# Optimization experiments

Hardware: AMD Instinct MI355X
Metric: run time of the kernel (lower is better)

Reference implementation:

```python
import jax, jax.numpy as jnp
import numpy as np

B, T, E, A = 8, 2048, 1024, 1024


def setup_inputs() -> dict:
    key = jax.random.key(0)
    k1, k2, k3, k4 = jax.random.split(key, 4)
    embedded = jax.random.normal(k1, (B, T, E), dtype=jnp.float32)
    s = 1.0 / np.sqrt(E)
    # nn.Linear(E, A, bias=False) stores weight of shape (A, E); y = x @ W^T
    Wq = jax.random.uniform(k2, (A, E), dtype=jnp.float32, minval=-s, maxval=s)
    Wk = jax.random.uniform(k3, (A, E), dtype=jnp.float32, minval=-s, maxval=s)
    Wv = jax.random.uniform(k4, (A, E), dtype=jnp.float32, minval=-s, maxval=s)
    return {"embedded": embedded, "Wq": Wq, "Wk": Wk, "Wv": Wv}


def reference(embedded, Wq, Wk, Wv):
    # q, k, v: [B, T, A]
    q = jnp.einsum("bte,ae->bta", embedded, Wq)
    k = jnp.einsum("bte,ae->bta", embedded, Wk)
    v = jnp.einsum("bte,ae->bta", embedded, Wv)
    scale = 1.0 / jnp.sqrt(jnp.asarray(Wq.shape[0], dtype=q.dtype))
    # causal scores: [B, T, T]
    scores = jnp.einsum("bqa,bka->bqk", q, k) * scale
    t = scores.shape[-1]
    causal = jnp.tril(jnp.ones((t, t), dtype=bool))
    scores = jnp.where(causal, scores, jnp.asarray(-jnp.inf, dtype=scores.dtype))
    attn = jax.nn.softmax(scores, axis=-1)
    return jnp.einsum("bqk,bka->bqa", attn, v)
```

## Files before the change

kernel.cpp:

```cpp
#include <hip/hip_runtime.h>
#include <hip/hip_bf16.h>
#include <stdint.h>


#define BB 8
#define TT 2048
#define EE 1024
#define AA 1024
#define MM (BB * TT)

typedef short bf16x8 __attribute__((ext_vector_type(8)));
typedef float f32x4 __attribute__((ext_vector_type(4)));

#define GLOAD_LDS16(g, l)                                                      \
  __builtin_amdgcn_global_load_lds(                                            \
      (const __attribute__((address_space(1))) void*)(g),                      \
      (__attribute__((address_space(3))) void*)(l), 16, 0, 0)

#define SBAR()                               \
  do {                                       \
    __builtin_amdgcn_sched_barrier(0);       \
    __builtin_amdgcn_s_barrier();            \
    __builtin_amdgcn_sched_barrier(0);       \
  } while (0)

#define LGKM0()                                          \
  do {                                                   \
    asm volatile("s_waitcnt lgkmcnt(0)" ::: "memory");   \
    __builtin_amdgcn_sched_barrier(0);                   \
  } while (0)

#define VMCNT(n)                                              \
  do {                                                        \
    asm volatile("s_waitcnt vmcnt(" #n ")" ::: "memory");     \
    __builtin_amdgcn_sched_barrier(0);                        \
  } while (0)

__device__ __forceinline__ void gemm256_core(
    const short* __restrict__ gA, int lda, int a0row,
    const short* __restrict__ gB, int ldb, int b0row, int NT, short* As,
    short* Bs, f32x4 (*acc)[4]) {
  const int tid = threadIdx.x;
  const int lane = tid & 63;
  const int w = tid >> 6;
  const int wr = w >> 2, wc = w & 3;
  const int lrow = lane & 15;
  const int lk8 = (lane >> 4) * 8;
  const int swz = ((lrow >> 3) & 1) << 4;
  const int baseA = (((wr * 128 + lrow) * 32) + lk8) ^ swz;
  const int baseB = (((wc * 64 + lrow) * 32) + lk8) ^ swz;

  const short* pA[2];
  const short* pB[2];
  int dL[2];
#pragma unroll
  for (int i = 0; i < 2; ++i) {
    int chunk = 2 * w + i;
    int P = chunk * 1024 + lane * 16;
    int L = P ^ (((P >> 9) & 1) << 5);
    int row = L >> 6;
    int kb2 = (L & 63) >> 1;
    pA[i] = gA + (size_t)(a0row + row) * lda + kb2;
    pB[i] = gB + (size_t)(b0row + row) * ldb + kb2;
    dL[i] = chunk * 512 + lane * 8;
  }

#define STG_A(tl, s)                                                           \
  do {                                                                         \
    int _o = (tl) * 64 + (s) * 32;                                             \
    short* _d = As + (((tl) & 1) << 14) + ((s) << 13);                         \
    GLOAD_LDS16(pA[0] + _o, _d + dL[0]);                                       \
    GLOAD_LDS16(pA[1] + _o, _d + dL[1]);                                       \
  } while (0)
#define STG_B(tl, s)                                                           \
  do {                                                                         \
    int _o = (tl) * 64 + (s) * 32;                                             \
    short* _d = Bs + (((tl) & 1) << 14) + ((s) << 13);                         \
    GLOAD_LDS16(pB[0] + _o, _d + dL[0]);                                       \
    GLOAD_LDS16(pB[1] + _o, _d + dL[1]);                                       \
  } while (0)

  STG_B(0, 0); STG_A(0, 0); STG_B(0, 1); STG_A(0, 1);
  if (NT > 1) {
    STG_B(1, 0); STG_A(1, 0); STG_A(1, 1);
    VMCNT(6);
  } else {
    VMCNT(0);
  }
  SBAR();

  for (int t = 0; t < NT; ++t) {
    short* Ac = As + (t & 1) * 16384;
    short* Bc = Bs + (t & 1) * 16384;
    const bool stg = (t < NT - 2);
    bf16x8 a0[4], a1[4], a2[4], a3[4], b0[4], b1[4];

#pragma unroll
    for (int m = 0; m < 4; ++m) a0[m] = *(const bf16x8*)&Ac[baseA + m * 512];
#pragma unroll
    for (int n = 0; n < 4; ++n) b0[n] = *(const bf16x8*)&Bc[baseB + n * 512];
    if (t < NT - 1) STG_B(t + 1, 1);
    SBAR();
    LGKM0();
    __builtin_amdgcn_s_setprio(1);
#pragma unroll
    for (int m = 0; m < 4; ++m)
#pragma unroll
      for (int n = 0; n < 4; ++n)
        acc[m][n] = __builtin_amdgcn_mfma_f32_16x16x32_bf16(a0[m], b0[n],
                                                            acc[m][n], 0, 0, 0);
    __builtin_amdgcn_s_setprio(0);
    SBAR();

#pragma unroll
    for (int m = 0; m < 4; ++m)
      a1[m] = *(const bf16x8*)&Ac[baseA + (m + 4) * 512];
#pragma unroll
    for (int m = 0; m < 4; ++m)
      a2[m] = *(const bf16x8*)&Ac[8192 + baseA + m * 512];
    if (stg) STG_B(t + 2, 0);
    SBAR();
    LGKM0();
    __builtin_amdgcn_s_setprio(1);
#pragma unroll
    for (int m = 0; m < 4; ++m)
#pragma unroll
      for (int n = 0; n < 4; ++n)
        acc[m + 4][n] = __builtin_amdgcn_mfma_f32_16x16x32_bf16(
            a1[m], b0[n], acc[m + 4][n], 0, 0, 0);
    __builtin_amdgcn_s_setprio(0);
    SBAR();

#pragma unroll
    for (int m = 0; m < 4; ++m)
      a3[m] = *(const bf16x8*)&Ac[8192 + baseA + (m + 4) * 512];
#pragma unroll
    for (int n = 0; n < 4; ++n)
      b1[n] = *(const bf16x8*)&Bc[8192 + baseB + n * 512];
    if (stg) STG_A(t + 2, 0);
    SBAR();
    LGKM0();
    __builtin_amdgcn_s_setprio(1);
#pragma unroll
    for (int m = 0; m < 4; ++m)
#pragma unroll
      for (int n = 0; n < 4; ++n)
        acc[m][n] = __builtin_amdgcn_mfma_f32_16x16x32_bf16(a2[m], b1[n],
                                                            acc[m][n], 0, 0, 0);
    __builtin_amdgcn_s_setprio(0);
    SBAR();

    if (stg) {
      STG_A(t + 2, 1);
      VMCNT(6);
    } else if (t == NT - 2) {
      VMCNT(0);
    }
    SBAR();
    __builtin_amdgcn_s_setprio(1);
#pragma unroll
    for (int m = 0; m < 4; ++m)
#pragma unroll
      for (int n = 0; n < 4; ++n)
        acc[m + 4][n] = __builtin_amdgcn_mfma_f32_16x16x32_bf16(
            a3[m], b1[n], acc[m + 4][n], 0, 0, 0);
    __builtin_amdgcn_s_setprio(0);
    SBAR();
  }
#undef STG_A
#undef STG_B
}

__global__ __launch_bounds__(512, 2) void qkv_gemm8(
    const short* __restrict__ xb, const short* __restrict__ Wb,
    short* __restrict__ qk, short* __restrict__ Vt) {
  __shared__ __align__(16) short SH[65536];
  short* As = SH;
  short* Bs = SH + 32768;
  int f = blockIdx.x;
  int s = (f & 7) * 96 + (f >> 3);
  int mt = s / 12, nt = s % 12;
  int z = nt >> 2, ntl = nt & 3;
  const short* gB = Wb + (size_t)z * AA * EE + (size_t)(ntl * 256) * EE;
  f32x4 acc[8][4];
#pragma unroll
  for (int m = 0; m < 8; ++m)
#pragma unroll
    for (int n = 0; n < 4; ++n) acc[m][n] = (f32x4){0.f, 0.f, 0.f, 0.f};
  gemm256_core(xb, EE, mt * 256, gB, EE, 0, EE / 64, As, Bs, acc);

  int tid = threadIdx.x;
  int lane = tid & 63, w = tid >> 6, wr = w >> 2, wc = w & 3;
  int lrow = lane & 15, lk4 = (lane >> 4) * 4;

  if (z < 2) {
    short* o = qk + (size_t)z * MM * AA;
    int row0 = mt * 256 + wr * 128;
    int col0 = ntl * 256 + wc * 64;
#pragma unroll
    for (int m = 0; m < 8; ++m)
#pragma unroll
      for (int n = 0; n < 4; ++n)
#pragma unroll
        for (int r = 0; r < 4; ++r) {
          int row = row0 + m * 16 + lk4 + r;
          int col = col0 + n * 16 + lrow;
          __hip_bfloat16 h = __float2bfloat16(acc[m][n][r]);
          o[(size_t)row * AA + col] = *(short*)&h;
        }
  } else {
    __syncthreads();
    int lr0 = wr * 128, lc0 = wc * 64;
#pragma unroll
    for (int m = 0; m < 8; ++m)
#pragma unroll
      for (int n = 0; n < 4; ++n)
#pragma unroll
        for (int r = 0; r < 4; ++r) {
          int lr = lr0 + m * 16 + lk4 + r;
          int lc = lc0 + n * 16 + lrow;
          __hip_bfloat16 h = __float2bfloat16(acc[m][n][r]);
          SH[lc * 256 + (lr ^ ((lc & 7) << 3))] = *(short*)&h;
        }
    __syncthreads();
    int row0 = mt * 256;
    int bq = row0 >> 11;
    int t0 = row0 & 2047;
#pragma unroll
    for (int pass = 0; pass < 4; ++pass) {
      int lc = pass * 64 + (tid >> 3);
      int d = ntl * 256 + lc;
      size_t dst = ((size_t)bq * AA + d) * TT + t0;
      int sw = (lc & 7) << 3;
#pragma unroll
      for (int g = 0; g < 4; ++g) {
        int lr = (tid & 7) * 8 + g * 64;
        bf16x8 vv = *(const bf16x8*)&SH[lc * 256 + (lr ^ sw)];
        *(bf16x8*)&Vt[dst + lr] = vv;
      }
    }
  }
}

__device__ __forceinline__ void stage_tile(const short* __restrict__ g,
                                           size_t stride, short* lds, int tid) {
#pragma unroll
  for (int r = 0; r < 4; ++r) {
    int t = r * 256 + tid;
    int row = t >> 3;
    int c = (t & 7) * 8;
    GLOAD_LDS16(g + (size_t)row * stride + c, lds + (size_t)t * 8);
  }
}

__device__ __forceinline__ void mfma_step(const short* As, const short* Bs,
                                          f32x4 acc[4][4], int lane, int wr,
                                          int wc) {
  int lrow = lane & 15;
  int lk = (lane >> 4) * 8;
#pragma unroll
  for (int kk = 0; kk < 64; kk += 32) {
    bf16x8 a[4], b[4];
#pragma unroll
    for (int i = 0; i < 4; ++i)
      a[i] = *(const bf16x8*)&As[(wr * 64 + i * 16 + lrow) * 64 + kk + lk];
#pragma unroll
    for (int j = 0; j < 4; ++j)
      b[j] = *(const bf16x8*)&Bs[(wc * 64 + j * 16 + lrow) * 64 + kk + lk];
#pragma unroll
    for (int i = 0; i < 4; ++i)
#pragma unroll
      for (int j = 0; j < 4; ++j)
        acc[i][j] =
            __builtin_amdgcn_mfma_f32_16x16x32_bf16(a[i], b[j], acc[i][j], 0, 0, 0);
  }
}

__global__ void prep(const float* __restrict__ x, const float* __restrict__ wq,
                     const float* __restrict__ wk, const float* __restrict__ wv,
                     short* __restrict__ Xb, short* __restrict__ Wb,
                     float* __restrict__ Ls) {
  const int nx4 = MM * EE / 4;
  const int nw4 = AA * EE / 4;
  int gid = blockIdx.x * blockDim.x + threadIdx.x;
  if (gid < MM) Ls[gid] = 0.f;
  int stride = gridDim.x * blockDim.x;
  for (int i = gid; i < nx4 + 3 * nw4; i += stride) {
    const float* src;
    short* dst;
    int ii;
    if (i < nx4) {
      src = x; dst = Xb; ii = i;
    } else {
      int j = i - nx4;
      int z = j / nw4;
      ii = j - z * nw4;
      src = (z == 0) ? wq : (z == 1 ? wk : wv);
      dst = Wb + (size_t)z * AA * EE;
    }
    float4 v = ((const float4*)src)[ii];
    __hip_bfloat16 h0 = __float2bfloat16(v.x);
    __hip_bfloat16 h1 = __float2bfloat16(v.y);
    __hip_bfloat16 h2 = __float2bfloat16(v.z);
    __hip_bfloat16 h3 = __float2bfloat16(v.w);
    short4 o;
    o.x = *(short*)&h0;
    o.y = *(short*)&h1;
    o.z = *(short*)&h2;
    o.w = *(short*)&h3;
    ((short4*)dst)[ii] = o;
  }
}

__global__ __launch_bounds__(256) void score_gemm(const short* __restrict__ Qb,
                                                  const short* __restrict__ Kb,
                                                  short* __restrict__ Pu,
                                                  float* __restrict__ lsum) {
  int f = blockIdx.x;
  int b = f & 7;
  int j = f >> 3;
  int mt = 0;
  while ((mt + 1) * (mt + 2) / 2 <= j) ++mt;
  int nt = j - mt * (mt + 1) / 2;
  int q0 = mt * 128, c0 = nt * 128;

  __shared__ __align__(16) short As[128 * 64];
  __shared__ __align__(16) short Bs[128 * 64];
  int tid = threadIdx.x;
  int lane = tid & 63, wid = tid >> 6, wr = wid >> 1, wc = wid & 1;
  const short* Q = Qb + (size_t)b * TT * AA;
  const short* K = Kb + (size_t)b * TT * AA;
  f32x4 acc[4][4];
#pragma unroll
  for (int i = 0; i < 4; ++i)
#pragma unroll
    for (int jj = 0; jj < 4; ++jj) acc[i][jj] = (f32x4){0.f, 0.f, 0.f, 0.f};

  for (int k0 = 0; k0 < AA; k0 += 64) {
    stage_tile(Q + (size_t)q0 * AA + k0, AA, As, tid);
    stage_tile(K + (size_t)c0 * AA + k0, AA, Bs, tid);
    __syncthreads();
    mfma_step(As, Bs, acc, lane, wr, wc);
    __syncthreads();
  }
  const float scale = 0.03125f;
  short* P = Pu + (size_t)b * TT * TT;
  int lrow = lane & 15, lk4 = (lane >> 4) * 4;
#pragma unroll
  for (int i = 0; i < 4; ++i) {
#pragma unroll
    for (int r = 0; r < 4; ++r) {
      int q = q0 + wr * 64 + i * 16 + lk4 + r;
      float rs = 0.f;
#pragma unroll
      for (int jj = 0; jj < 4; ++jj) {
        int kx = c0 + wc * 64 + jj * 16 + lrow;
        float e = (kx <= q) ? __expf(acc[i][jj][r] * scale) : 0.f;
        rs += e;
        __hip_bfloat16 h = __float2bfloat16(e);
        P[(size_t)q * TT + kx] = *(short*)&h;
      }
      rs += __shfl_xor(rs, 1);
      rs += __shfl_xor(rs, 2);
      rs += __shfl_xor(rs, 4);
      rs += __shfl_xor(rs, 8);
      if (lrow == 0) atomicAdd(&lsum[b * TT + q], rs);
    }
  }
}

__global__ __launch_bounds__(256) void pv_gemm(const short* __restrict__ Pu,
                                               const short* __restrict__ Vt,
                                               const float* __restrict__ lsum,
                                               float* __restrict__ out) {
  int f = blockIdx.x;
  int b = f & 7;
  int j = f >> 3;
  int p = j >> 3;
  int nt = j & 7;
  int n0 = nt * 128;

  __shared__ __align__(16) short As[128 * 64];
  __shared__ __align__(16) short Bs[128 * 64];
  int tid = threadIdx.x;
  int lane = tid & 63, wid = tid >> 6, wr = wid >> 1, wc = wid & 1;
  const short* P = Pu + (size_t)b * TT * TT;
  const short* V = Vt + (size_t)b * AA * TT;
  int lrow = lane & 15, lk4 = (lane >> 4) * 4;

#pragma unroll
  for (int s = 0; s < 2; ++s) {
    int mt = s ? (15 - p) : p;
    int q0 = mt * 128;
    f32x4 acc[4][4];
#pragma unroll
    for (int i = 0; i < 4; ++i)
#pragma unroll
      for (int jj = 0; jj < 4; ++jj) acc[i][jj] = (f32x4){0.f, 0.f, 0.f, 0.f};

    int kend = q0 + 128;
    for (int k0 = 0; k0 < kend; k0 += 64) {
      stage_tile(P + (size_t)q0 * TT + k0, TT, As, tid);
      stage_tile(V + (size_t)n0 * TT + k0, TT, Bs, tid);
      __syncthreads();
      mfma_step(As, Bs, acc, lane, wr, wc);
      __syncthreads();
    }
#pragma unroll
    for (int i = 0; i < 4; ++i) {
#pragma unroll
      for (int r = 0; r < 4; ++r) {
        int q = q0 + wr * 64 + i * 16 + lk4 + r;
        float linv = 1.0f / lsum[b * TT + q];
#pragma unroll
        for (int jj = 0; jj < 4; ++jj) {
          int d = n0 + wc * 64 + jj * 16 + lrow;
          out[((size_t)(b * TT + q)) * AA + d] = acc[i][jj][r] * linv;
        }
      }
    }
  }
}

extern "C" void kernel_launch(void* const* d_in, const int* in_sizes, int n_in,
                              void* d_out, int out_size, void* d_ws,
                              size_t ws_size, hipStream_t stream) {
  const float* x = (const float*)d_in[0];
  const float* Wq = (const float*)d_in[1];
  const float* Wk = (const float*)d_in[2];
  const float* Wv = (const float*)d_in[3];

  char* ws = (char*)d_ws;
  size_t oWb = 0;
  size_t oQb = oWb + (size_t)3 * AA * EE * 2;
  size_t oKb = oQb + (size_t)MM * AA * 2;
  size_t oVt = oKb + (size_t)MM * AA * 2;
  size_t oLs = oVt + (size_t)MM * AA * 2;
  size_t oXb = oLs + (size_t)MM * 4;
  size_t oPu = oXb;

  short* Wb = (short*)(ws + oWb);
  short* Qb = (short*)(ws + oQb);
  short* Kb = (short*)(ws + oKb);
  short* Vt = (short*)(ws + oVt);
  float* Ls = (float*)(ws + oLs);
  short* Xb = (short*)(ws + oXb);
  short* Pu = (short*)(ws + oPu);

  prep<<<2048, 256, 0, stream>>>(x, Wq, Wk, Wv, Xb, Wb, Ls);

  qkv_gemm8<<<768, 512, 0, stream>>>(Xb, Wb, Qb, Vt);
  score_gemm<<<1088, 256, 0, stream>>>(Qb, Kb, Pu, Ls);
  pv_gemm<<<512, 256, 0, stream>>>(Pu, Vt, Ls, (float*)d_out);
}
```

Measured before the change: 260.8 us.

## Split causal score GEMM into 256-tile off-diagonal and 128-tile diagonal kernels

The score computation is split in two. A new 256x256-tile kernel (512 threads, reusing gemm256_core) covers the strictly-below-diagonal blocks without masking, and a 128-tile kernel covers the three lower-triangle sub-tiles of each 256 diagonal block with the causal mask. The PV kernel now computes its paired short and long query tiles in one loop that shares the staged V tile, instead of running two sequential passes. This aims to raise data reuse and MFMA efficiency in the score phase and halve V loads in PV, at the cost of an extra launch and higher register and LDS pressure.

```diff
diff --git a/kernel.cpp b/kernel.cpp
--- a/kernel.cpp
+++ b/kernel.cpp
@@ -242,6 +242,56 @@
   }
 }
 
+__global__ __launch_bounds__(512, 2) void score256(const short* __restrict__ Qb,
+                                                   const short* __restrict__ Kb,
+                                                   short* __restrict__ Pu,
+                                                   float* __restrict__ lsum) {
+  __shared__ __align__(16) short As[32768];
+  __shared__ __align__(16) short Bs[32768];
+  int f = blockIdx.x;
+  int b = f & 7;
+  int j = f >> 3;
+  int MT = 1;
+  while ((MT + 1) * MT / 2 <= j) ++MT;
+  int NT = j - MT * (MT - 1) / 2;
+  const short* Q = Qb + (size_t)b * TT * AA;
+  const short* K = Kb + (size_t)b * TT * AA;
+  f32x4 acc[8][4];
+#pragma unroll
+  for (int m = 0; m < 8; ++m)
+#pragma unroll
+    for (int n = 0; n < 4; ++n) acc[m][n] = (f32x4){0.f, 0.f, 0.f, 0.f};
+  gemm256_core(Q, AA, MT * 256, K, AA, NT * 256, AA / 64, As, Bs, acc);
+
+  const float scale = 0.03125f;
+  short* P = Pu + (size_t)b * TT * TT;
+  int lane = threadIdx.x & 63, w = threadIdx.x >> 6, wr = w >> 2, wc = w & 3;
+  int lrow = lane & 15, lk4 = (lane >> 4) * 4;
+  int q0 = MT * 256 + wr * 128;
+  int c0 = NT * 256 + wc * 64;
+#pragma unroll
+  for (int m = 0; m < 8; ++m) {
+#pragma unroll
+    for (int r = 0; r < 4; ++r) {
+      int q = q0 + m * 16 + lk4 + r;
+      float rs = 0.f;
+#pragma unroll
+      for (int n = 0; n < 4; ++n) {
+        int kx = c0 + n * 16 + lrow;
+        float e = __expf(acc[m][n][r] * scale);
+        rs += e;
+        __hip_bfloat16 h = __float2bfloat16(e);
+        P[(size_t)q * TT + kx] = *(short*)&h;
+      }
+      rs += __shfl_xor(rs, 1);
+      rs += __shfl_xor(rs, 2);
+      rs += __shfl_xor(rs, 4);
+      rs += __shfl_xor(rs, 8);
+      if (lrow == 0) atomicAdd(&lsum[b * TT + q], rs);
+    }
+  }
+}
+
 __device__ __forceinline__ void stage_tile(const short* __restrict__ g,
                                            size_t stride, short* lds, int tid) {
 #pragma unroll
@@ -273,6 +323,125 @@
       for (int j = 0; j < 4; ++j)
         acc[i][j] =
             __builtin_amdgcn_mfma_f32_16x16x32_bf16(a[i], b[j], acc[i][j], 0, 0, 0);
+  }
+}
+
+__global__ __launch_bounds__(256) void score_diag(const short* __restrict__ Qb,
+                                                  const short* __restrict__ Kb,
+                                                  short* __restrict__ Pu,
+                                                  float* __restrict__ lsum) {
+  int f = blockIdx.x;
+  int b = f & 7;
+  int j = f >> 3;
+  int M = j / 3, r3 = j - 3 * M;
+  int mt = 2 * M + (r3 > 0);
+  int nt = 2 * M + (r3 == 2);
+  int q0 = mt * 128, c0 = nt * 128;
+
+  __shared__ __align__(16) short As[128 * 64];
+  __shared__ __align__(16) short Bs[128 * 64];
+  int tid = threadIdx.x;
+  int lane = tid & 63, wid = tid >> 6, wr = wid >> 1, wc = wid & 1;
+  const short* Q = Qb + (size_t)b * TT * AA;
+  const short* K = Kb + (size_t)b * TT * AA;
+  f32x4 acc[4][4];
+#pragma unroll
+  for (int i = 0; i < 4; ++i)
+#pragma unroll
+    for (int jj = 0; jj < 4; ++jj) acc[i][jj] = (f32x4){0.f, 0.f, 0.f, 0.f};
+
+  for (int k0 = 0; k0 < AA; k0 += 64) {
+    stage_tile(Q + (size_t)q0 * AA + k0, AA, As, tid);
+    stage_tile(K + (size_t)c0 * AA + k0, AA, Bs, tid);
+    __syncthreads();
+    mfma_step(As, Bs, acc, lane, wr, wc);
+    __syncthreads();
+  }
+  const float scale = 0.03125f;
+  short* P = Pu + (size_t)b * TT * TT;
+  int lrow = lane & 15, lk4 = (lane >> 4) * 4;
+#pragma unroll
+  for (int i = 0; i < 4; ++i) {
+#pragma unroll
+    for (int r = 0; r < 4; ++r) {
+      int q = q0 + wr * 64 + i * 16 + lk4 + r;
+      float rs = 0.f;
+#pragma unroll
+      for (int jj = 0; jj < 4; ++jj) {
+        int kx = c0 + wc * 64 + jj * 16 + lrow;
+        float e = (kx <= q) ? __expf(acc[i][jj][r] * scale) : 0.f;
+        rs += e;
+        __hip_bfloat16 h = __float2bfloat16(e);
+        P[(size_t)q * TT + kx] = *(short*)&h;
+      }
+      rs += __shfl_xor(rs, 1);
+      rs += __shfl_xor(rs, 2);
+      rs += __shfl_xor(rs, 4);
+      rs += __shfl_xor(rs, 8);
+      if (lrow == 0) atomicAdd(&lsum[b * TT + q], rs);
+    }
+  }
+}
+
+__global__ __launch_bounds__(256) void pv_gemm(const short* __restrict__ Pu,
+                                               const short* __restrict__ Vt,
+                                               const float* __restrict__ lsum,
+                                               float* __restrict__ out) {
+  int f = blockIdx.x;
+  int b = f & 7;
+  int j = f >> 3;
+  int pp = j >> 3;
+  int nt = j & 7;
+  int n0 = nt * 128;
+  int q0A = pp * 128;
+  int q0B = (15 - pp) * 128;
+  int e1 = 2 * (pp + 1);
+  int e2 = 2 * (16 - pp);
+
+  __shared__ __align__(16) short A1[128 * 64];
+  __shared__ __align__(16) short A2[128 * 64];
+  __shared__ __align__(16) short BV[128 * 64];
+  int tid = threadIdx.x;
+  int lane = tid & 63, wid = tid >> 6, wr = wid >> 1, wc = wid & 1;
+  const short* P = Pu + (size_t)b * TT * TT;
+  const short* V = Vt + (size_t)b * AA * TT;
+  int lrow = lane & 15, lk4 = (lane >> 4) * 4;
+
+  f32x4 accA[4][4], accB[4][4];
+#pragma unroll
+  for (int i = 0; i < 4; ++i)
+#pragma unroll
+    for (int jj = 0; jj < 4; ++jj) {
+      accA[i][jj] = (f32x4){0.f, 0.f, 0.f, 0.f};
+      accB[i][jj] = (f32x4){0.f, 0.f, 0.f, 0.f};
+    }
+
+  for (int k = 0; k < e2; ++k) {
+    int k0 = k * 64;
+    stage_tile(V + (size_t)n0 * TT + k0, TT, BV, tid);
+    stage_tile(P + (size_t)q0B * TT + k0, TT, A2, tid);
+    if (k < e1) stage_tile(P + (size_t)q0A * TT + k0, TT, A1, tid);
+    __syncthreads();
+    mfma_step(A2, BV, accB, lane, wr, wc);
+    if (k < e1) mfma_step(A1, BV, accA, lane, wr, wc);
+    __syncthreads();
+  }
+
+#pragma unroll
+  for (int i = 0; i < 4; ++i) {
+#pragma unroll
+    for (int r = 0; r < 4; ++r) {
+      int qA = q0A + wr * 64 + i * 16 + lk4 + r;
+      int qB = q0B + wr * 64 + i * 16 + lk4 + r;
+      float lA = 1.0f / lsum[b * TT + qA];
+      float lB = 1.0f / lsum[b * TT + qB];
+#pragma unroll
+      for (int jj = 0; jj < 4; ++jj) {
+        int d = n0 + wc * 64 + jj * 16 + lrow;
+        out[((size_t)(b * TT + qA)) * AA + d] = accA[i][jj][r] * lA;
+        out[((size_t)(b * TT + qB)) * AA + d] = accB[i][jj][r] * lB;
+      }
+    }
   }
 }
 
@@ -312,116 +481,6 @@
   }
 }
 
-__global__ __launch_bounds__(256) void score_gemm(const short* __restrict__ Qb,
-                                                  const short* __restrict__ Kb,
-                                                  short* __restrict__ Pu,
-                                                  float* __restrict__ lsum) {
-  int f = blockIdx.x;
-  int b = f & 7;
-  int j = f >> 3;
-  int mt = 0;
-  while ((mt + 1) * (mt + 2) / 2 <= j) ++mt;
-  int nt = j - mt * (mt + 1) / 2;
-  int q0 = mt * 128, c0 = nt * 128;
-
-  __shared__ __align__(16) short As[128 * 64];
-  __shared__ __align__(16) short Bs[128 * 64];
-  int tid = threadIdx.x;
-  int lane = tid & 63, wid = tid >> 6, wr = wid >> 1, wc = wid & 1;
-  const short* Q = Qb + (size_t)b * TT * AA;
-  const short* K = Kb + (size_t)b * TT * AA;
-  f32x4 acc[4][4];
-#pragma unroll
-  for (int i = 0; i < 4; ++i)
-#pragma unroll
-    for (int jj = 0; jj < 4; ++jj) acc[i][jj] = (f32x4){0.f, 0.f, 0.f, 0.f};
-
-  for (int k0 = 0; k0 < AA; k0 += 64) {
-    stage_tile(Q + (size_t)q0 * AA + k0, AA, As, tid);
-    stage_tile(K + (size_t)c0 * AA + k0, AA, Bs, tid);
-    __syncthreads();
-    mfma_step(As, Bs, acc, lane, wr, wc);
-    __syncthreads();
-  }
-  const float scale = 0.03125f;
-  short* P = Pu + (size_t)b * TT * TT;
-  int lrow = lane & 15, lk4 = (lane >> 4) * 4;
-#pragma unroll
-  for (int i = 0; i < 4; ++i) {
-#pragma unroll
-    for (int r = 0; r < 4; ++r) {
-      int q = q0 + wr * 64 + i * 16 + lk4 + r;
-      float rs = 0.f;
-#pragma unroll
-      for (int jj = 0; jj < 4; ++jj) {
-        int kx = c0 + wc * 64 + jj * 16 + lrow;
-        float e = (kx <= q) ? __expf(acc[i][jj][r] * scale) : 0.f;
-        rs += e;
-        __hip_bfloat16 h = __float2bfloat16(e);
-        P[(size_t)q * TT + kx] = *(short*)&h;
-      }
-      rs += __shfl_xor(rs, 1);
-      rs += __shfl_xor(rs, 2);
-      rs += __shfl_xor(rs, 4);
-      rs += __shfl_xor(rs, 8);
-      if (lrow == 0) atomicAdd(&lsum[b * TT + q], rs);
-    }
-  }
-}
-
-__global__ __launch_bounds__(256) void pv_gemm(const short* __restrict__ Pu,
-                                               const short* __restrict__ Vt,
-                                               const float* __restrict__ lsum,
-                                               float* __restrict__ out) {
-  int f = blockIdx.x;
-  int b = f & 7;
-  int j = f >> 3;
-  int p = j >> 3;
-  int nt = j & 7;
-  int n0 = nt * 128;
-
-  __shared__ __align__(16) short As[128 * 64];
-  __shared__ __align__(16) short Bs[128 * 64];
-  int tid = threadIdx.x;
-  int lane = tid & 63, wid = tid >> 6, wr = wid >> 1, wc = wid & 1;
-  const short* P = Pu + (size_t)b * TT * TT;
-  const short* V = Vt + (size_t)b * AA * TT;
-  int lrow = lane & 15, lk4 = (lane >> 4) * 4;
-
-#pragma unroll
-  for (int s = 0; s < 2; ++s) {
-    int mt = s ? (15 - p) : p;
-    int q0 = mt * 128;
-    f32x4 acc[4][4];
-#pragma unroll
-    for (int i = 0; i < 4; ++i)
-#pragma unroll
-      for (int jj = 0; jj < 4; ++jj) acc[i][jj] = (f32x4){0.f, 0.f, 0.f, 0.f};
-
-    int kend = q0 + 128;
-    for (int k0 = 0; k0 < kend; k0 += 64) {
-      stage_tile(P + (size_t)q0 * TT + k0, TT, As, tid);
-      stage_tile(V + (size_t)n0 * TT + k0, TT, Bs, tid);
-      __syncthreads();
-      mfma_step(As, Bs, acc, lane, wr, wc);
-      __syncthreads();
-    }
-#pragma unroll
-    for (int i = 0; i < 4; ++i) {
-#pragma unroll
-      for (int r = 0; r < 4; ++r) {
-        int q = q0 + wr * 64 + i * 16 + lk4 + r;
-        float linv = 1.0f / lsum[b * TT + q];
-#pragma unroll
-        for (int jj = 0; jj < 4; ++jj) {
-          int d = n0 + wc * 64 + jj * 16 + lrow;
-          out[((size_t)(b * TT + q)) * AA + d] = acc[i][jj][r] * linv;
-        }
-      }
-    }
-  }
-}
-
 extern "C" void kernel_launch(void* const* d_in, const int* in_sizes, int n_in,
                               void* d_out, int out_size, void* d_ws,
                               size_t ws_size, hipStream_t stream) {
@@ -450,6 +509,7 @@
   prep<<<2048, 256, 0, stream>>>(x, Wq, Wk, Wv, Xb, Wb, Ls);
 
   qkv_gemm8<<<768, 512, 0, stream>>>(Xb, Wb, Qb, Vt);
-  score_gemm<<<1088, 256, 0, stream>>>(Qb, Kb, Pu, Ls);
+  score256<<<224, 512, 0, stream>>>(Qb, Kb, Pu, Ls);
+  score_diag<<<192, 256, 0, stream>>>(Qb, Kb, Pu, Ls);
   pv_gemm<<<512, 256, 0, stream>>>(Pu, Vt, Ls, (float*)d_out);
 }
```

After: 272.9 us. 4.6% more time.
